# Performance work log

Measured on AMD Instinct MI355X. Metric: run time of the kernel, lower is better.

Reference implementation:

```python
import jax, jax.numpy as jnp
import numpy as np

N_NODES = 100000

def setup_inputs() -> dict:
    key = jax.random.key(0)
    k1, k2, k3, k4 = jax.random.split(key, 4)
    feat = jax.random.normal(k1, (N_NODES, 256), dtype=jnp.float32)
    # xavier_uniform for [256,256]: bound = sqrt(6/(256+256))
    bound = float(np.sqrt(6.0 / (256 + 256)))
    weight1 = jax.random.uniform(k2, (256, 256), dtype=jnp.float32, minval=-bound, maxval=bound)
    src = jax.random.randint(k3, (1600000,), 0, N_NODES, dtype=jnp.int64)
    dst = jax.random.randint(k4, (1600000,), 0, N_NODES, dtype=jnp.int64)
    return {"feat": feat, "weight1": weight1, "src": src, "dst": dst}

def reference(feat, weight1, src, dst):
    # Per-etype copy_src + scatter-sum accumulated across etypes == one
    # segment_sum over the union of all edges (norm is computed but unused
    # in the original _apply).
    agg = jax.ops.segment_sum(feat[src], dst, num_segments=N_NODES)  # [N, d]
    h = (agg + feat) @ weight1
    h = jax.nn.relu(h)
    # F.dropout(training=False) is identity
    return h
```

## Files before the change

### kernel.cpp

```cpp
#include <hip/hip_runtime.h>

#define D 256
#define CAP 32
#define MAXOVF 4096
#define BM 64

#define RN 32
#define RSH 5
#define SCAP 1024
#define PCH 8192
#define PTH 512
#define NRANGES_MAX 4096
#define SGT 256

typedef float f32x4 __attribute__((ext_vector_type(4)));
typedef short s16x8 __attribute__((ext_vector_type(8)));

__device__ inline unsigned int f2bf(float x) {
    unsigned int u = __float_as_uint(x);
    return (u + 0x7FFFu + ((u >> 16) & 1u)) >> 16;
}
__device__ inline float bflo(unsigned int u) { return __uint_as_float(u << 16); }
__device__ inline float bfhi(unsigned int u) { return __uint_as_float(u & 0xFFFF0000u); }

__device__ inline void gload16(const char* g, const unsigned char* lds) {
    __builtin_amdgcn_global_load_lds(
        (const __attribute__((address_space(1))) void*)g,
        (__attribute__((address_space(3))) void*)lds, 16, 0, 0);
}

__global__ __launch_bounds__(256) void k_pre(const float* __restrict__ feat,
                                             unsigned short* __restrict__ featb,
                                             const float* __restrict__ W,
                                             unsigned short* __restrict__ wTs,
                                             int* __restrict__ gcur, int nz, long n8) {
    const int bid = blockIdx.x;
    const int t = threadIdx.x;
    if (bid < 256) {
        unsigned short v = (unsigned short)f2bf(W[(size_t)t * D + bid]);
        int ks = t >> 5;
        int byte = ((bid << 6) + (((t >> 3) & 3) << 4) + ((t & 7) << 1)) ^ ((bid & 7) << 4);
        *reinterpret_cast<unsigned short*>(
            reinterpret_cast<char*>(wTs) + (size_t)ks * 16384 + byte) = v;
    } else if (bid < 272) {
        int i = (bid - 256) * 256 + t;
        if (i < nz) gcur[i] = 0;
    }
    for (long i = bid * 256L + t; i < n8; i += (long)gridDim.x * 256) {
        const float4* p = reinterpret_cast<const float4*>(feat + i * 8);
        float4 a = p[0], b = p[1];
        uint4 u;
        u.x = f2bf(a.x) | (f2bf(a.y) << 16);
        u.y = f2bf(a.z) | (f2bf(a.w) << 16);
        u.z = f2bf(b.x) | (f2bf(b.y) << 16);
        u.w = f2bf(b.z) | (f2bf(b.w) << 16);
        reinterpret_cast<uint4*>(featb)[i] = u;
    }
}


__global__ void k_zero(int* __restrict__ p, int n) {
    int i = blockIdx.x * blockDim.x + threadIdx.x;
    if (i < n) p[i] = 0;
}

__global__ __launch_bounds__(256) void k_f2b(const float* __restrict__ f,
                                             unsigned short* __restrict__ fb, long n8) {
    for (long i = blockIdx.x * 256L + threadIdx.x; i < n8; i += (long)gridDim.x * 256) {
        const float4* p = reinterpret_cast<const float4*>(f + i * 8);
        float4 a = p[0], b = p[1];
        uint4 u;
        u.x = f2bf(a.x) | (f2bf(a.y) << 16);
        u.y = f2bf(a.z) | (f2bf(a.w) << 16);
        u.z = f2bf(b.x) | (f2bf(b.y) << 16);
        u.w = f2bf(b.z) | (f2bf(b.w) << 16);
        reinterpret_cast<uint4*>(fb)[i] = u;
    }
}

__global__ __launch_bounds__(256) void k_wTs(const float* __restrict__ W,
                                             unsigned short* __restrict__ wTs) {
    int col = blockIdx.x;
    int k = threadIdx.x;
    unsigned short v = (unsigned short)f2bf(W[(size_t)k * D + col]);
    int ks = k >> 5;
    int byte = ((col << 6) + (((k >> 3) & 3) << 4) + ((k & 7) << 1)) ^ ((col & 7) << 4);
    *reinterpret_cast<unsigned short*>(
        reinterpret_cast<char*>(wTs) + (size_t)ks * 16384 + byte) = v;
}

__global__ __launch_bounds__(PTH) void k_part(const int* __restrict__ src,
                                              const int* __restrict__ dst,
                                              int* __restrict__ gcur,
                                              int* __restrict__ streams,
                                              int* __restrict__ ovf,
                                              int* __restrict__ ovf_cnt,
                                              int E, int nranges) {
    __shared__ int hist[NRANGES_MAX];
    __shared__ int base[NRANGES_MAX];
    __shared__ int off[NRANGES_MAX];
    const int t = threadIdx.x;
    const long e0 = (long)blockIdx.x * PCH;
    for (int i = t; i < nranges; i += PTH) hist[i] = 0;
    __syncthreads();
    int md[PCH / PTH], ms[PCH / PTH];
    #pragma unroll
    for (int i = 0; i < PCH / PTH; ++i) {
        long e = e0 + (long)i * PTH + t;
        if (e < E) {
            md[i] = dst[e];
            ms[i] = src[e];
            atomicAdd(&hist[md[i] >> RSH], 1);
        } else {
            md[i] = -1;
        }
    }
    __syncthreads();
    for (int i = t; i < nranges; i += PTH) {
        int h = hist[i];
        base[i] = h ? atomicAdd(&gcur[i], h) : 0;
        off[i] = 0;
    }
    __syncthreads();
    #pragma unroll
    for (int i = 0; i < PCH / PTH; ++i) {
        if (md[i] >= 0) {
            int r = md[i] >> RSH;
            int p = base[r] + atomicAdd(&off[r], 1);
            if (p < SCAP) {
                streams[(size_t)r * SCAP + p] = (ms[i] << RSH) | (md[i] & (RN - 1));
            } else {
                int o = atomicAdd(ovf_cnt, 1);
                if (o < MAXOVF) { ovf[2 * o] = ms[i]; ovf[2 * o + 1] = md[i]; }
            }
        }
    }
}

__global__ __launch_bounds__(SGT) void k_sgg(const unsigned short* __restrict__ featb,
                                             const int* __restrict__ gcur,
                                             const int* __restrict__ streams,
                                             const int* __restrict__ ovf,
                                             const int* __restrict__ ovf_cnt,
                                             const unsigned short* __restrict__ wTs,
                                             float* __restrict__ out, int N) {
    __shared__ int hist[RN], basei[RN], off[RN], scn[RN];
    __shared__ int elist[SCAP];
    __shared__ __align__(16) unsigned char s_agg[RN * 512];
    const int r = blockIdx.x;
    const int t = threadIdx.x;
    const int node0 = r << RSH;
    const int wv = t >> 6;
    const int l = t & 63;
    const char* wb = reinterpret_cast<const char*>(wTs);

    int cnt = gcur[r];
    if (cnt > SCAP) cnt = SCAP;
    if (t < RN) { hist[t] = 0; off[t] = 0; }
    __syncthreads();
    int ent[SCAP / SGT];
    #pragma unroll
    for (int i = 0; i < SCAP / SGT; ++i) {
        int p = t + i * SGT;
        if (p < cnt) {
            ent[i] = streams[(size_t)r * SCAP + p];
            atomicAdd(&hist[ent[i] & (RN - 1)], 1);
        } else {
            ent[i] = -1;
        }
    }
    __syncthreads();
    if (t < RN) scn[t] = hist[t];
    __syncthreads();
    for (int st = 1; st < RN; st <<= 1) {
        int v = 0;
        if (t < RN && t >= st) v = scn[t - st];
        __syncthreads();
        if (t < RN) scn[t] += v;
        __syncthreads();
    }
    if (t < RN) basei[t] = scn[t] - hist[t];
    __syncthreads();
    #pragma unroll
    for (int i = 0; i < SCAP / SGT; ++i) {
        if (ent[i] >= 0) {
            int ln_ = ent[i] & (RN - 1);
            int p = basei[ln_] + atomicAdd(&off[ln_], 1);
            elist[p] = ent[i] >> RSH;
        }
    }
    __syncthreads();

    int ovfn = *ovf_cnt;
    if (ovfn > MAXOVF) ovfn = MAXOVF;
    for (int k = 0; k < RN / 4; ++k) {
        int ln_ = wv * (RN / 4) + k;
        int node = node0 + ln_;
        unsigned short* rowp = reinterpret_cast<unsigned short*>(s_agg) + ln_ * 256;
        int us = (l * 4) ^ ((ln_ & 7) << 3);
        if (node >= N) {
            uint2 z; z.x = 0; z.y = 0;
            *reinterpret_cast<uint2*>(rowp + us) = z;
            continue;
        }
        int cb = hist[ln_];
        int bb = basei[ln_];
        uint2 u = reinterpret_cast<const uint2*>(featb + (size_t)node * D)[l];
        float4 acc;
        acc.x = bflo(u.x); acc.y = bfhi(u.x); acc.z = bflo(u.y); acc.w = bfhi(u.y);
        int j = 0;
        for (; j + 16 <= cb; j += 16) {
            int s[16];
            #pragma unroll
            for (int q = 0; q < 16; ++q) s[q] = elist[bb + j + q];
            uint2 v[16];
            #pragma unroll
            for (int q = 0; q < 16; ++q)
                v[q] = reinterpret_cast<const uint2*>(featb + (size_t)s[q] * D)[l];
            #pragma unroll
            for (int q = 0; q < 16; ++q) {
                acc.x += bflo(v[q].x); acc.y += bfhi(v[q].x);
                acc.z += bflo(v[q].y); acc.w += bfhi(v[q].y);
            }
        }
        for (; j + 8 <= cb; j += 8) {
            int s[8];
            #pragma unroll
            for (int q = 0; q < 8; ++q) s[q] = elist[bb + j + q];
            uint2 v[8];
            #pragma unroll
            for (int q = 0; q < 8; ++q)
                v[q] = reinterpret_cast<const uint2*>(featb + (size_t)s[q] * D)[l];
            #pragma unroll
            for (int q = 0; q < 8; ++q) {
                acc.x += bflo(v[q].x); acc.y += bfhi(v[q].x);
                acc.z += bflo(v[q].y); acc.w += bfhi(v[q].y);
            }
        }
        for (; j < cb; ++j) {
            uint2 v = reinterpret_cast<const uint2*>(featb + (size_t)elist[bb + j] * D)[l];
            acc.x += bflo(v.x); acc.y += bfhi(v.x);
            acc.z += bflo(v.y); acc.w += bfhi(v.y);
        }
        if (ovfn > 0) {
            for (int e = 0; e < ovfn; ++e) {
                if (ovf[2 * e + 1] == node) {
                    uint2 v = reinterpret_cast<const uint2*>(featb + (size_t)ovf[2 * e] * D)[l];
                    acc.x += bflo(v.x); acc.y += bfhi(v.x);
                    acc.z += bflo(v.y); acc.w += bfhi(v.y);
                }
            }
        }
        uint2 w;
        w.x = f2bf(acc.x) | (f2bf(acc.y) << 16);
        w.y = f2bf(acc.z) | (f2bf(acc.w) << 16);
        *reinterpret_cast<uint2*>(rowp + us) = w;
    }
    __syncthreads();

    f32x4 acc[2][4];
    #pragma unroll
    for (int rt = 0; rt < 2; ++rt)
        #pragma unroll
        for (int ct = 0; ct < 4; ++ct) acc[rt][ct] = (f32x4){0.f, 0.f, 0.f, 0.f};

    const int g = l >> 4;
    const int cl = l & 15;
    #pragma unroll
    for (int ks = 0; ks < 8; ++ks) {
        const int kb = ks * 32 + g * 8;
        s16x8 bf[4];
        #pragma unroll
        for (int ct = 0; ct < 4; ++ct) {
            int col = wv * 64 + ct * 16 + cl;
            int bb = (col * 64 + g * 16) ^ ((col & 7) << 4);
            bf[ct] = *reinterpret_cast<const s16x8*>(wb + (size_t)ks * 16384 + bb);
        }
        s16x8 af[2];
        #pragma unroll
        for (int rt = 0; rt < 2; ++rt) {
            int lr = rt * 16 + cl;
            int ab = (lr * 512 + kb * 2) ^ ((lr & 7) << 4);
            af[rt] = *reinterpret_cast<const s16x8*>(s_agg + ab);
        }
        #pragma unroll
        for (int ct = 0; ct < 4; ++ct) {
            acc[0][ct] = __builtin_amdgcn_mfma_f32_16x16x32_bf16(af[0], bf[ct], acc[0][ct], 0, 0, 0);
            acc[1][ct] = __builtin_amdgcn_mfma_f32_16x16x32_bf16(af[1], bf[ct], acc[1][ct], 0, 0, 0);
        }
    }

    #pragma unroll
    for (int rt = 0; rt < 2; ++rt) {
        #pragma unroll
        for (int ct = 0; ct < 4; ++ct) {
            #pragma unroll
            for (int rr = 0; rr < 4; ++rr) {
                int row = node0 + rt * 16 + (l >> 4) * 4 + rr;
                int col = wv * 64 + ct * 16 + cl;
                if (row < N)
                    out[(size_t)row * D + col] = fmaxf(acc[rt][ct][rr], 0.f);
            }
        }
    }
}

__global__ void k_fillcap(const int* __restrict__ src, const int* __restrict__ dst,
                          int* __restrict__ counts, int* __restrict__ buckets,
                          int* __restrict__ ovf, int* __restrict__ ovf_cnt, int E) {
    for (int e = blockIdx.x * blockDim.x + threadIdx.x; e < E;
         e += gridDim.x * blockDim.x) {
        int d = dst[e];
        int pos = atomicAdd(&counts[d], 1);
        if (pos < CAP) {
            buckets[(size_t)d * CAP + pos] = src[e];
        } else {
            int o = atomicAdd(ovf_cnt, 1);
            if (o < MAXOVF) {
                ovf[2 * o + 0] = src[e];
                ovf[2 * o + 1] = d;
            }
        }
    }
}


#define GAT_BODY(LOAD, ACCUM)                                                  \
    int j = 0;                                                                 \
    for (; j + 16 <= cnt; j += 16) {                                           \
        int s[16];                                                             \
        _Pragma("unroll") for (int q = 0; q < 16; ++q) s[q] = bk[j + q];       \
        LOAD(16)                                                               \
        ACCUM(16)                                                              \
    }                                                                          \
    for (; j + 8 <= cnt; j += 8) {                                             \
        int s[8];                                                              \
        _Pragma("unroll") for (int q = 0; q < 8; ++q) s[q] = bk[j + q];        \
        LOAD(8)                                                                \
        ACCUM(8)                                                               \
    }

__global__ __launch_bounds__(256) void g_bf_aggb(const unsigned short* __restrict__ fb,
                                                 const int* __restrict__ counts,
                                                 const int* __restrict__ buckets,
                                                 const int* __restrict__ ovf,
                                                 const int* __restrict__ ovf_cnt,
                                                 unsigned short* __restrict__ aggb, int N) {
    int node = (int)((blockIdx.x * (long)blockDim.x + threadIdx.x) >> 6);
    int ln = threadIdx.x & 63;
    if (node >= N) return;
    int cnt_raw = counts[node];
    int cnt = cnt_raw > CAP ? CAP : cnt_raw;
    const int* bk = buckets + (size_t)node * CAP;
    uint2 u = reinterpret_cast<const uint2*>(fb + (size_t)node * D)[ln];
    float4 acc;
    acc.x = bflo(u.x); acc.y = bfhi(u.x); acc.z = bflo(u.y); acc.w = bfhi(u.y);
#define BLOAD(W_)                                                              \
    uint2 v[W_];                                                               \
    _Pragma("unroll") for (int q = 0; q < W_; ++q)                             \
        v[q] = reinterpret_cast<const uint2*>(fb + (size_t)s[q] * D)[ln];
#define BACC(W_)                                                               \
    _Pragma("unroll") for (int q = 0; q < W_; ++q) {                           \
        acc.x += bflo(v[q].x); acc.y += bfhi(v[q].x);                          \
        acc.z += bflo(v[q].y); acc.w += bfhi(v[q].y);                          \
    }
    GAT_BODY(BLOAD, BACC)
    for (; j < cnt; ++j) {
        uint2 v = reinterpret_cast<const uint2*>(fb + (size_t)bk[j] * D)[ln];
        acc.x += bflo(v.x); acc.y += bfhi(v.x);
        acc.z += bflo(v.y); acc.w += bfhi(v.y);
    }
    if (cnt_raw > CAP) {
        int m = *ovf_cnt;
        if (m > MAXOVF) m = MAXOVF;
        for (int e = 0; e < m; ++e) {
            if (ovf[2 * e + 1] == node) {
                uint2 v = reinterpret_cast<const uint2*>(fb + (size_t)ovf[2 * e] * D)[ln];
                acc.x += bflo(v.x); acc.y += bfhi(v.x);
                acc.z += bflo(v.y); acc.w += bfhi(v.y);
            }
        }
    }
    uint2 w;
    w.x = f2bf(acc.x) | (f2bf(acc.y) << 16);
    w.y = f2bf(acc.z) | (f2bf(acc.w) << 16);
    unsigned short* rowp = aggb + (size_t)node * D;
    int us = (ln * 4) ^ ((node & 7) << 3);
    *reinterpret_cast<uint2*>(rowp + us) = w;
}

__global__ __launch_bounds__(256) void g_f32_out(const float* __restrict__ feat,
                                                 const int* __restrict__ counts,
                                                 const int* __restrict__ buckets,
                                                 const int* __restrict__ ovf,
                                                 const int* __restrict__ ovf_cnt,
                                                 float* __restrict__ out, int N) {
    int node = (int)((blockIdx.x * (long)blockDim.x + threadIdx.x) >> 6);
    int ln = threadIdx.x & 63;
    if (node >= N) return;
    int cnt_raw = counts[node];
    int cnt = cnt_raw > CAP ? CAP : cnt_raw;
    const int* bk = buckets + (size_t)node * CAP;
    float4 acc = reinterpret_cast<const float4*>(feat + (size_t)node * D)[ln];
#define FLOAD(W_)                                                              \
    float4 v[W_];                                                              \
    _Pragma("unroll") for (int q = 0; q < W_; ++q)                             \
        v[q] = reinterpret_cast<const float4*>(feat + (size_t)s[q] * D)[ln];
#define FACC(W_)                                                               \
    _Pragma("unroll") for (int q = 0; q < W_; ++q) {                           \
        acc.x += v[q].x; acc.y += v[q].y; acc.z += v[q].z; acc.w += v[q].w;    \
    }
    GAT_BODY(FLOAD, FACC)
    for (; j < cnt; ++j) {
        float4 v = reinterpret_cast<const float4*>(feat + (size_t)bk[j] * D)[ln];
        acc.x += v.x; acc.y += v.y; acc.z += v.z; acc.w += v.w;
    }
    if (cnt_raw > CAP) {
        int m = *ovf_cnt;
        if (m > MAXOVF) m = MAXOVF;
        for (int e = 0; e < m; ++e) {
            if (ovf[2 * e + 1] == node) {
                float4 v = reinterpret_cast<const float4*>(feat + (size_t)ovf[2 * e] * D)[ln];
                acc.x += v.x; acc.y += v.y; acc.z += v.z; acc.w += v.w;
            }
        }
    }
    reinterpret_cast<float4*>(out + (size_t)node * D)[ln] = acc;
}


__global__ __launch_bounds__(256) void gc_copy(const float* __restrict__ feat,
                                               float* __restrict__ agg, long n4) {
    long i = (long)blockIdx.x * blockDim.x + threadIdx.x;
    if (i < n4)
        reinterpret_cast<float4*>(agg)[i] = reinterpret_cast<const float4*>(feat)[i];
}

__global__ __launch_bounds__(256) void gc_scatter(const float* __restrict__ feat,
                                                  const int* __restrict__ src,
                                                  const int* __restrict__ dst,
                                                  float* __restrict__ agg, int n_edges) {
    int wave = (int)((blockIdx.x * (long)blockDim.x + threadIdx.x) >> 6);
    int lane = threadIdx.x & 63;
    if (wave >= n_edges) return;
    int s = src[wave];
    int d = dst[wave];
    const float4 v = reinterpret_cast<const float4*>(feat + (size_t)s * D)[lane];
    float* p = agg + (size_t)d * D + (size_t)lane * 4;
    atomicAdd(p + 0, v.x);
    atomicAdd(p + 1, v.y);
    atomicAdd(p + 2, v.z);
    atomicAdd(p + 3, v.w);
}


__global__ __launch_bounds__(256) void gemm_mfma_b(const unsigned short* __restrict__ aggb,
                                                   const unsigned short* __restrict__ wTs,
                                                   float* __restrict__ out, int n_rows) {
    __shared__ __align__(16) unsigned char s_a[BM * 512];
    __shared__ __align__(16) unsigned char s_b[16384];
    const int t = threadIdx.x;
    const int row0 = blockIdx.x * BM;
    const int wv = t >> 6;
    const int l = t & 63;
    const char* wb = reinterpret_cast<const char*>(wTs);

    const char* gbase = reinterpret_cast<const char*>(aggb) + (size_t)row0 * 512;
    #pragma unroll
    for (int q = 0; q < 8; ++q) {
        int off = wv * 8192 + q * 1024;
        gload16(gbase + off + l * 16, s_a + off);
    }
    #pragma unroll
    for (int i = 0; i < 4; ++i) {
        int off = wv * 4096 + i * 1024;
        gload16(wb + off + l * 16, s_b + off);
    }
    __syncthreads();

    f32x4 acc[16];
    #pragma unroll
    for (int ct = 0; ct < 16; ++ct) acc[ct] = (f32x4){0.f, 0.f, 0.f, 0.f};

    const int lr = wv * 16 + (l & 15);
    const int g = l >> 4;
    for (int ks = 0; ks < 8; ++ks) {
        const int kb = ks * 32 + g * 8;
        const int ab = (lr * 512 + kb * 2) ^ ((lr & 7) << 4);
        s16x8 af = *reinterpret_cast<const s16x8*>(s_a + ab);
        #pragma unroll
        for (int ct = 0; ct < 16; ++ct) {
            int col = ct * 16 + (l & 15);
            int bb = (col * 64 + g * 16) ^ ((col & 7) << 4);
            s16x8 bf = *reinterpret_cast<const s16x8*>(s_b + bb);
            acc[ct] = __builtin_amdgcn_mfma_f32_16x16x32_bf16(af, bf, acc[ct], 0, 0, 0);
        }
        __syncthreads();
        if (ks < 7) {
            #pragma unroll
            for (int i = 0; i < 4; ++i) {
                int off = wv * 4096 + i * 1024;
                gload16(wb + (size_t)(ks + 1) * 16384 + off + l * 16, s_b + off);
            }
            __syncthreads();
        }
    }

    const int rbase = row0 + wv * 16 + (l >> 4) * 4;
    const int cb = l & 15;
    #pragma unroll
    for (int ct = 0; ct < 16; ++ct) {
        #pragma unroll
        for (int r = 0; r < 4; ++r) {
            int row = rbase + r;
            if (row < n_rows)
                out[(size_t)row * D + ct * 16 + cb] = fmaxf(acc[ct][r], 0.f);
        }
    }
}

__global__ __launch_bounds__(256) void gemm_mfma(const unsigned short* __restrict__ wTs,
                                                 float* __restrict__ out, int n_rows) {
    __shared__ __align__(16) unsigned char s_a[BM * 512];
    __shared__ __align__(16) unsigned char s_b[16384];
    const int t = threadIdx.x;
    const int row0 = blockIdx.x * BM;
    const int wv = t >> 6;
    const int l = t & 63;
    const char* wb = reinterpret_cast<const char*>(wTs);

    #pragma unroll
    for (int i = 0; i < 4; ++i) {
        int off = wv * 4096 + i * 1024;
        gload16(wb + off + l * 16, s_b + off);
    }
    #pragma unroll
    for (int i = 0; i < 16; ++i) {
        int f4 = t + 256 * i;
        int row = f4 >> 6;
        int kc = f4 & 63;
        int grow = row0 + row;
        if (grow >= n_rows) grow = n_rows - 1;
        float4 v = *reinterpret_cast<const float4*>(out + (size_t)grow * D + kc * 4);
        uint2 u;
        u.x = f2bf(v.x) | (f2bf(v.y) << 16);
        u.y = f2bf(v.z) | (f2bf(v.w) << 16);
        int byte = (row * 512 + kc * 8) ^ ((row & 7) << 4);
        *reinterpret_cast<uint2*>(s_a + byte) = u;
    }
    __syncthreads();

    f32x4 acc[16];
    #pragma unroll
    for (int ct = 0; ct < 16; ++ct) acc[ct] = (f32x4){0.f, 0.f, 0.f, 0.f};

    const int lr = wv * 16 + (l & 15);
    const int g = l >> 4;
    for (int ks = 0; ks < 8; ++ks) {
        const int kb = ks * 32 + g * 8;
        const int ab = (lr * 512 + kb * 2) ^ ((lr & 7) << 4);
        s16x8 af = *reinterpret_cast<const s16x8*>(s_a + ab);
        #pragma unroll
        for (int ct = 0; ct < 16; ++ct) {
            int col = ct * 16 + (l & 15);
            int bb = (col * 64 + g * 16) ^ ((col & 7) << 4);
            s16x8 bf = *reinterpret_cast<const s16x8*>(s_b + bb);
            acc[ct] = __builtin_amdgcn_mfma_f32_16x16x32_bf16(af, bf, acc[ct], 0, 0, 0);
        }
        __syncthreads();
        if (ks < 7) {
            #pragma unroll
            for (int i = 0; i < 4; ++i) {
                int off = wv * 4096 + i * 1024;
                gload16(wb + (size_t)(ks + 1) * 16384 + off + l * 16, s_b + off);
            }
            __syncthreads();
        }
    }

    const int rbase = row0 + wv * 16 + (l >> 4) * 4;
    const int cb = l & 15;
    #pragma unroll
    for (int ct = 0; ct < 16; ++ct) {
        #pragma unroll
        for (int r = 0; r < 4; ++r) {
            int row = rbase + r;
            if (row < n_rows)
                out[(size_t)row * D + ct * 16 + cb] = fmaxf(acc[ct][r], 0.f);
        }
    }
}

__global__ __launch_bounds__(256) void gemm_relu(const float* __restrict__ Wm,
                                                 float* __restrict__ out, int n_rows) {
    __shared__ float s_a[32][D];
    const int row0 = blockIdx.x * 32;
    const int c = threadIdx.x;
    {
        const float4* gsrc = reinterpret_cast<const float4*>(out + (size_t)row0 * D);
        float4* ldst = reinterpret_cast<float4*>(&s_a[0][0]);
        #pragma unroll
        for (int i = 0; i < 8; ++i)
            ldst[threadIdx.x + i * 256] = gsrc[threadIdx.x + i * 256];
    }
    __syncthreads();
    float acc[32];
    #pragma unroll
    for (int r = 0; r < 32; ++r) acc[r] = 0.f;
    #pragma unroll 4
    for (int k = 0; k < D; ++k) {
        float w = Wm[(size_t)k * D + c];
        #pragma unroll
        for (int r = 0; r < 32; ++r) acc[r] += s_a[r][k] * w;
    }
    #pragma unroll
    for (int r = 0; r < 32; ++r) {
        int row = row0 + r;
        if (row < n_rows) out[(size_t)row * D + c] = fmaxf(acc[r], 0.f);
    }
}

extern "C" void kernel_launch(void* const* d_in, const int* in_sizes, int n_in,
                              void* d_out, int out_size, void* d_ws, size_t ws_size,
                              hipStream_t stream) {
    const float* feat = (const float*)d_in[0];
    const float* W    = (const float*)d_in[1];
    const int*   src  = (const int*)d_in[2];
    const int*   dst  = (const int*)d_in[3];
    float* out = (float*)d_out;

    const int N = in_sizes[0] / D;
    const int E = in_sizes[2];
    const int Npad = ((N + BM - 1) / BM) * BM;
    auto al = [](size_t x) { return (x + 255) & ~(size_t)255; };

    const int nranges = (N + RN - 1) / RN;
    const int gemm_blocks = (N + BM - 1) / BM;
    const int gat_blocks = (N + 3) / 4;

    const size_t hdr_bytes   = ((size_t)nranges + 1 + 2 * MAXOVF) * 4;
    const size_t strm_off    = al(hdr_bytes);
    const size_t strm_sz     = (size_t)nranges * SCAP * 4;
    const size_t a2_featb_off = al(strm_off + strm_sz);
    const size_t featb_sz    = (size_t)N * D * 2;
    const size_t a2_wt_off   = al(a2_featb_off + featb_sz);
    const size_t wt_sz       = (size_t)D * D * 2;
    const size_t need_A2     = a2_wt_off + wt_sz;

    const size_t cap_bytes = ((size_t)N + 1 + 2 * MAXOVF + (size_t)N * CAP) * 4;
    const size_t featb_off = al(cap_bytes);
    const size_t wt_off    = al(featb_off + featb_sz);
    const size_t aggb_off  = al(wt_off + wt_sz);
    const size_t aggb_sz   = (size_t)Npad * D * 2;
    const size_t need_A    = aggb_off + aggb_sz;

    if (ws_size >= need_A2 && nranges <= NRANGES_MAX) {
        char* base = (char*)d_ws;
        int* gcur    = (int*)base;
        int* ovf_cnt = gcur + nranges;
        int* ovf     = ovf_cnt + 1;
        int* streams = (int*)(base + strm_off);
        unsigned short* featb = (unsigned short*)(base + a2_featb_off);
        unsigned short* wTs   = (unsigned short*)(base + a2_wt_off);

        k_pre<<<2048, 256, 0, stream>>>(feat, featb, W, wTs, gcur, nranges + 1,
                                        (long)N * D / 8);
        k_part<<<(E + PCH - 1) / PCH, PTH, 0, stream>>>(src, dst, gcur, streams,
                                                        ovf, ovf_cnt, E, nranges);
        k_sgg<<<nranges, SGT, 0, stream>>>(featb, gcur, streams, ovf, ovf_cnt,
                                           wTs, out, N);
    } else if (ws_size >= need_A) {
        char* base = (char*)d_ws;
        int* counts  = (int*)base;
        int* ovf_cnt = counts + N;
        int* ovf     = ovf_cnt + 1;
        int* buckets = ovf + 2 * MAXOVF;
        unsigned short* featb = (unsigned short*)(base + featb_off);
        unsigned short* wTs   = (unsigned short*)(base + wt_off);
        unsigned short* aggb  = (unsigned short*)(base + aggb_off);

        k_zero<<<(N + 1 + 255) / 256, 256, 0, stream>>>(counts, N + 1);
        k_f2b<<<2048, 256, 0, stream>>>(feat, featb, (long)N * D / 8);
        k_wTs<<<D, 256, 0, stream>>>(W, wTs);
        k_fillcap<<<2048, 256, 0, stream>>>(src, dst, counts, buckets, ovf, ovf_cnt, E);
        g_bf_aggb<<<gat_blocks, 256, 0, stream>>>(featb, counts, buckets, ovf, ovf_cnt, aggb, N);
        gemm_mfma_b<<<gemm_blocks, 256, 0, stream>>>(aggb, wTs, out, N);
    } else if (ws_size >= cap_bytes) {
        char* base = (char*)d_ws;
        int* counts  = (int*)base;
        int* ovf_cnt = counts + N;
        int* ovf     = ovf_cnt + 1;
        int* buckets = ovf + 2 * MAXOVF;
        unsigned short* wTs = (unsigned short*)(((uintptr_t)buckets + 255) & ~(uintptr_t)255);

        k_zero<<<(N + 1 + 255) / 256, 256, 0, stream>>>(counts, N + 1);
        k_fillcap<<<2048, 256, 0, stream>>>(src, dst, counts, buckets, ovf, ovf_cnt, E);
        g_f32_out<<<gat_blocks, 256, 0, stream>>>(feat, counts, buckets, ovf, ovf_cnt, out, N);
        k_wTs<<<D, 256, 0, stream>>>(W, wTs);
        gemm_mfma<<<gemm_blocks, 256, 0, stream>>>(wTs, out, N);
    } else {
        long n4 = (long)N * D / 4;
        gc_copy<<<(int)((n4 + 255) / 256), 256, 0, stream>>>(feat, out, n4);
        gc_scatter<<<(E + 3) / 4, 256, 0, stream>>>(feat, src, dst, out, E);
        gemm_relu<<<(N + 31) / 32, 256, 0, stream>>>(W, out, N);
    }
}
```

Baseline: 212.5 us.

## Fuse edge partitioning with bf16 feature and weight conversion into one launch

The separate preprocessing kernel (feature and weight bf16 conversion plus counter zeroing) and the edge-partition kernel are merged into one 2048-block, 512-thread kernel. Different block ranges do edge partitioning, weight transpose, and feature conversion. Counter zeroing moves to a hipMemsetAsync, because the partition blocks now need the counters cleared before they start. This removes a kernel boundary and lets the memory-bound conversion overlap the atomic-heavy partitioning. In exchange, every block reserves 48KB of shared memory, even the blocks that only convert features, which can reduce occupancy for the conversion work.

```diff
diff --git a/kernel.cpp b/kernel.cpp
--- a/kernel.cpp
+++ b/kernel.cpp
@@ -9,9 +9,9 @@
 #define RSH 5
 #define SCAP 1024
 #define PCH 8192
-#define PTH 512
 #define NRANGES_MAX 4096
 #define SGT 256
+#define NPP 2048
 
 typedef float f32x4 __attribute__((ext_vector_type(4)));
 typedef short s16x8 __attribute__((ext_vector_type(8)));
@@ -29,110 +29,80 @@
         (__attribute__((address_space(3))) void*)lds, 16, 0, 0);
 }
 
-__global__ __launch_bounds__(256) void k_pre(const float* __restrict__ feat,
-                                             unsigned short* __restrict__ featb,
-                                             const float* __restrict__ W,
-                                             unsigned short* __restrict__ wTs,
-                                             int* __restrict__ gcur, int nz, long n8) {
-    const int bid = blockIdx.x;
-    const int t = threadIdx.x;
-    if (bid < 256) {
-        unsigned short v = (unsigned short)f2bf(W[(size_t)t * D + bid]);
-        int ks = t >> 5;
-        int byte = ((bid << 6) + (((t >> 3) & 3) << 4) + ((t & 7) << 1)) ^ ((bid & 7) << 4);
-        *reinterpret_cast<unsigned short*>(
-            reinterpret_cast<char*>(wTs) + (size_t)ks * 16384 + byte) = v;
-    } else if (bid < 272) {
-        int i = (bid - 256) * 256 + t;
-        if (i < nz) gcur[i] = 0;
-    }
-    for (long i = bid * 256L + t; i < n8; i += (long)gridDim.x * 256) {
-        const float4* p = reinterpret_cast<const float4*>(feat + i * 8);
-        float4 a = p[0], b = p[1];
-        uint4 u;
-        u.x = f2bf(a.x) | (f2bf(a.y) << 16);
-        u.y = f2bf(a.z) | (f2bf(a.w) << 16);
-        u.z = f2bf(b.x) | (f2bf(b.y) << 16);
-        u.w = f2bf(b.z) | (f2bf(b.w) << 16);
-        reinterpret_cast<uint4*>(featb)[i] = u;
-    }
-}
-
-
-__global__ void k_zero(int* __restrict__ p, int n) {
-    int i = blockIdx.x * blockDim.x + threadIdx.x;
-    if (i < n) p[i] = 0;
-}
-
-__global__ __launch_bounds__(256) void k_f2b(const float* __restrict__ f,
-                                             unsigned short* __restrict__ fb, long n8) {
-    for (long i = blockIdx.x * 256L + threadIdx.x; i < n8; i += (long)gridDim.x * 256) {
-        const float4* p = reinterpret_cast<const float4*>(f + i * 8);
-        float4 a = p[0], b = p[1];
-        uint4 u;
-        u.x = f2bf(a.x) | (f2bf(a.y) << 16);
-        u.y = f2bf(a.z) | (f2bf(a.w) << 16);
-        u.z = f2bf(b.x) | (f2bf(b.y) << 16);
-        u.w = f2bf(b.z) | (f2bf(b.w) << 16);
-        reinterpret_cast<uint4*>(fb)[i] = u;
-    }
-}
-
-__global__ __launch_bounds__(256) void k_wTs(const float* __restrict__ W,
-                                             unsigned short* __restrict__ wTs) {
-    int col = blockIdx.x;
-    int k = threadIdx.x;
-    unsigned short v = (unsigned short)f2bf(W[(size_t)k * D + col]);
-    int ks = k >> 5;
-    int byte = ((col << 6) + (((k >> 3) & 3) << 4) + ((k & 7) << 1)) ^ ((col & 7) << 4);
-    *reinterpret_cast<unsigned short*>(
-        reinterpret_cast<char*>(wTs) + (size_t)ks * 16384 + byte) = v;
-}
-
-__global__ __launch_bounds__(PTH) void k_part(const int* __restrict__ src,
-                                              const int* __restrict__ dst,
-                                              int* __restrict__ gcur,
-                                              int* __restrict__ streams,
-                                              int* __restrict__ ovf,
-                                              int* __restrict__ ovf_cnt,
-                                              int E, int nranges) {
+__global__ __launch_bounds__(512) void k_pp(const float* __restrict__ feat,
+                                            unsigned short* __restrict__ featb,
+                                            const float* __restrict__ W,
+                                            unsigned short* __restrict__ wTs,
+                                            const int* __restrict__ src,
+                                            const int* __restrict__ dst,
+                                            int* __restrict__ gcur,
+                                            int* __restrict__ streams,
+                                            int* __restrict__ ovf,
+                                            int* __restrict__ ovf_cnt,
+                                            int E, int nranges, long n8) {
     __shared__ int hist[NRANGES_MAX];
     __shared__ int base[NRANGES_MAX];
     __shared__ int off[NRANGES_MAX];
+    const int bid = blockIdx.x;
     const int t = threadIdx.x;
-    const long e0 = (long)blockIdx.x * PCH;
-    for (int i = t; i < nranges; i += PTH) hist[i] = 0;
-    __syncthreads();
-    int md[PCH / PTH], ms[PCH / PTH];
-    #pragma unroll
-    for (int i = 0; i < PCH / PTH; ++i) {
-        long e = e0 + (long)i * PTH + t;
-        if (e < E) {
-            md[i] = dst[e];
-            ms[i] = src[e];
-            atomicAdd(&hist[md[i] >> RSH], 1);
-        } else {
-            md[i] = -1;
-        }
-    }
-    __syncthreads();
-    for (int i = t; i < nranges; i += PTH) {
-        int h = hist[i];
-        base[i] = h ? atomicAdd(&gcur[i], h) : 0;
-        off[i] = 0;
-    }
-    __syncthreads();
-    #pragma unroll
-    for (int i = 0; i < PCH / PTH; ++i) {
-        if (md[i] >= 0) {
-            int r = md[i] >> RSH;
-            int p = base[r] + atomicAdd(&off[r], 1);
-            if (p < SCAP) {
-                streams[(size_t)r * SCAP + p] = (ms[i] << RSH) | (md[i] & (RN - 1));
+    const int nparts = (E + PCH - 1) / PCH;
+
+    if (bid < nparts) {
+        const long e0 = (long)bid * PCH;
+        for (int i = t; i < nranges; i += 512) hist[i] = 0;
+        __syncthreads();
+        int md[PCH / 512], ms[PCH / 512];
+        #pragma unroll
+        for (int i = 0; i < PCH / 512; ++i) {
+            long e = e0 + (long)i * 512 + t;
+            if (e < E) {
+                md[i] = dst[e];
+                ms[i] = src[e];
+                atomicAdd(&hist[md[i] >> RSH], 1);
             } else {
-                int o = atomicAdd(ovf_cnt, 1);
-                if (o < MAXOVF) { ovf[2 * o] = ms[i]; ovf[2 * o + 1] = md[i]; }
-            }
+                md[i] = -1;
+            }
+        }
+        __syncthreads();
+        for (int i = t; i < nranges; i += 512) {
+            int h = hist[i];
+            base[i] = h ? atomicAdd(&gcur[i], h) : 0;
+            off[i] = 0;
+        }
+        __syncthreads();
+        #pragma unroll
+        for (int i = 0; i < PCH / 512; ++i) {
+            if (md[i] >= 0) {
+                int r = md[i] >> RSH;
+                int p = base[r] + atomicAdd(&off[r], 1);
+                if (p < SCAP) {
+                    streams[(size_t)r * SCAP + p] = (ms[i] << RSH) | (md[i] & (RN - 1));
+                } else {
+                    int o = atomicAdd(ovf_cnt, 1);
+                    if (o < MAXOVF) { ovf[2 * o] = ms[i]; ovf[2 * o + 1] = md[i]; }
+                }
+            }
+        }
+    } else if (bid < nparts + 128) {
+        int col = (bid - nparts) * 2 + (t >> 8);
+        int k = t & 255;
+        unsigned short v = (unsigned short)f2bf(W[(size_t)k * D + col]);
+        int ks = k >> 5;
+        int byte = ((col << 6) + (((k >> 3) & 3) << 4) + ((k & 7) << 1)) ^ ((col & 7) << 4);
+        *reinterpret_cast<unsigned short*>(
+            reinterpret_cast<char*>(wTs) + (size_t)ks * 16384 + byte) = v;
+    } else {
+        const long fbid = bid - nparts - 128;
+        const long nfb = NPP - nparts - 128;
+        for (long i = fbid * 512 + t; i < n8; i += nfb * 512) {
+            const float4* p = reinterpret_cast<const float4*>(feat + i * 8);
+            float4 a = p[0], b = p[1];
+            uint4 u;
+            u.x = f2bf(a.x) | (f2bf(a.y) << 16);
+            u.y = f2bf(a.z) | (f2bf(a.w) << 16);
+            u.z = f2bf(b.x) | (f2bf(b.y) << 16);
+            u.w = f2bf(b.z) | (f2bf(b.w) << 16);
+            reinterpret_cast<uint4*>(featb)[i] = u;
         }
     }
 }
@@ -305,6 +275,37 @@
     }
 }
 
+
+__global__ void k_zero(int* __restrict__ p, int n) {
+    int i = blockIdx.x * blockDim.x + threadIdx.x;
+    if (i < n) p[i] = 0;
+}
+
+__global__ __launch_bounds__(256) void k_f2b(const float* __restrict__ f,
+                                             unsigned short* __restrict__ fb, long n8) {
+    for (long i = blockIdx.x * 256L + threadIdx.x; i < n8; i += (long)gridDim.x * 256) {
+        const float4* p = reinterpret_cast<const float4*>(f + i * 8);
+        float4 a = p[0], b = p[1];
+        uint4 u;
+        u.x = f2bf(a.x) | (f2bf(a.y) << 16);
+        u.y = f2bf(a.z) | (f2bf(a.w) << 16);
+        u.z = f2bf(b.x) | (f2bf(b.y) << 16);
+        u.w = f2bf(b.z) | (f2bf(b.w) << 16);
+        reinterpret_cast<uint4*>(fb)[i] = u;
+    }
+}
+
+__global__ __launch_bounds__(256) void k_wTs(const float* __restrict__ W,
+                                             unsigned short* __restrict__ wTs) {
+    int col = blockIdx.x;
+    int k = threadIdx.x;
+    unsigned short v = (unsigned short)f2bf(W[(size_t)k * D + col]);
+    int ks = k >> 5;
+    int byte = ((col << 6) + (((k >> 3) & 3) << 4) + ((k & 7) << 1)) ^ ((col & 7) << 4);
+    *reinterpret_cast<unsigned short*>(
+        reinterpret_cast<char*>(wTs) + (size_t)ks * 16384 + byte) = v;
+}
+
 __global__ void k_fillcap(const int* __restrict__ src, const int* __restrict__ dst,
                           int* __restrict__ counts, int* __restrict__ buckets,
                           int* __restrict__ ovf, int* __restrict__ ovf_cnt, int E) {
@@ -323,7 +324,6 @@
         }
     }
 }
-
 
 #define GAT_BODY(LOAD, ACCUM)                                                  \
     int j = 0;                                                                 \
@@ -428,7 +428,6 @@
     reinterpret_cast<float4*>(out + (size_t)node * D)[ln] = acc;
 }
 
-
 __global__ __launch_bounds__(256) void gc_copy(const float* __restrict__ feat,
                                                float* __restrict__ agg, long n4) {
     long i = (long)blockIdx.x * blockDim.x + threadIdx.x;
@@ -453,7 +452,6 @@
     atomicAdd(p + 3, v.w);
 }
 
-
 __global__ __launch_bounds__(256) void gemm_mfma_b(const unsigned short* __restrict__ aggb,
                                                    const unsigned short* __restrict__ wTs,
                                                    float* __restrict__ out, int n_rows) {
@@ -635,6 +633,7 @@
     auto al = [](size_t x) { return (x + 255) & ~(size_t)255; };
 
     const int nranges = (N + RN - 1) / RN;
+    const int nparts = (E + PCH - 1) / PCH;
     const int gemm_blocks = (N + BM - 1) / BM;
     const int gat_blocks = (N + 3) / 4;
 
@@ -654,7 +653,8 @@
     const size_t aggb_sz   = (size_t)Npad * D * 2;
     const size_t need_A    = aggb_off + aggb_sz;
 
-    if (ws_size >= need_A2 && nranges <= NRANGES_MAX) {
+    if (ws_size >= need_A2 && nranges <= NRANGES_MAX &&
+        nparts + 128 + 256 <= NPP) {
         char* base = (char*)d_ws;
         int* gcur    = (int*)base;
         int* ovf_cnt = gcur + nranges;
@@ -663,10 +663,10 @@
         unsigned short* featb = (unsigned short*)(base + a2_featb_off);
         unsigned short* wTs   = (unsigned short*)(base + a2_wt_off);
 
-        k_pre<<<2048, 256, 0, stream>>>(feat, featb, W, wTs, gcur, nranges + 1,
-                                        (long)N * D / 8);
-        k_part<<<(E + PCH - 1) / PCH, PTH, 0, stream>>>(src, dst, gcur, streams,
-                                                        ovf, ovf_cnt, E, nranges);
+        hipMemsetAsync(gcur, 0, ((size_t)nranges + 1) * 4, stream);
+        k_pp<<<NPP, 512, 0, stream>>>(feat, featb, W, wTs, src, dst, gcur,
+                                      streams, ovf, ovf_cnt, E, nranges,
+                                      (long)N * D / 8);
         k_sgg<<<nranges, SGT, 0, stream>>>(featb, gcur, streams, ovf, ovf_cnt,
                                            wTs, out, N);
     } else if (ws_size >= need_A) {
```

Result: faster. 206.4 us (-2.9%).
